# Kernel optimization log

Measured on AMD Instinct MI355X. Metric: run time of the kernel, lower is better.

## Reference

```python
import jax, jax.numpy as jnp
import numpy as np

B, N, H, DH, CZ = 1, 768, 16, 32, 128
D = H * DH  # 512
EPS = 1e-5


def layer_norm(x, w, b):
    mu = jnp.mean(x, axis=-1, keepdims=True)
    var = jnp.var(x, axis=-1, keepdims=True)
    return (x - mu) * jax.lax.rsqrt(var + EPS) * w + b


def setup_inputs() -> dict:
    key = jax.random.key(0)
    ks = jax.random.split(key, 10)
    sc = 0.02
    return {
        "s": jax.random.normal(ks[0], (B, N, D), jnp.float32),
        "z": jax.random.normal(ks[1], (B, N, N, CZ), jnp.float32),
        "norm_s_w": jnp.ones((D,), jnp.float32),
        "norm_s_b": jnp.zeros((D,), jnp.float32),
        "q_w": jax.random.normal(ks[2], (D, D), jnp.float32) * sc,
        "q_b": jax.random.normal(ks[3], (D,), jnp.float32) * sc,
        "k_w": jax.random.normal(ks[4], (D, D), jnp.float32) * sc,
        "v_w": jax.random.normal(ks[5], (D, D), jnp.float32) * sc,
        "g_w": jax.random.normal(ks[6], (D, D), jnp.float32) * sc,
        "zn_w": jnp.ones((CZ,), jnp.float32),
        "zn_b": jnp.zeros((CZ,), jnp.float32),
        "z_w": jax.random.normal(ks[7], (CZ, H), jnp.float32) * sc,
        "o_w": jax.random.normal(ks[8], (D, D), jnp.float32) * sc,
    }


def reference(s, z, norm_s_w, norm_s_b, q_w, q_b, k_w, v_w, g_w, zn_w, zn_b, z_w, o_w):
    # initial_norm on s
    s_n = layer_norm(s, norm_s_w, norm_s_b)
    # QKV projections (q has bias, k/v do not)
    q = (s_n @ q_w + q_b).reshape(B, N, H, DH)
    k = (s_n @ k_w).reshape(B, N, H, DH)
    v = (s_n @ v_w).reshape(B, N, H, DH)
    # attention scores [B, H, N, N]
    scores = jnp.einsum("bihd,bjhd->bhij", q, k) * (DH ** -0.5)
    # pair bias: layernorm(z) then linear c_z -> H, permute to [B, H, N, N]
    z_bias = layer_norm(z, zn_w, zn_b) @ z_w            # [B, N, N, H]
    z_bias = jnp.transpose(z_bias, (0, 3, 1, 2))         # [B, H, N, N]
    a = jax.nn.softmax(scores + z_bias, axis=-1)
    # attend
    o = jnp.einsum("bhij,bjhd->bihd", a, v).reshape(B, N, D)
    # sigmoid gate from normed s
    g = jax.nn.sigmoid(s_n @ g_w)
    # output projection
    return (o * g) @ o_w
```

## Files before the change

### kernel.cpp

```cpp
#include <hip/hip_runtime.h>
#include <hip/hip_bf16.h>

typedef float f32x4 __attribute__((ext_vector_type(4)));
typedef short bf16x8 __attribute__((ext_vector_type(8)));
typedef unsigned short u16;

#define NTOK 768
#define DMOD 512
#define NH   16
#define DH   32
#define CZd  128
#define NN   (768*768)

static __device__ __forceinline__ u16 f2bf(float f) {
  __hip_bfloat16 h = __float2bfloat16(f);
  return __builtin_bit_cast(u16, h);
}
static __device__ __forceinline__ float bf2f(u16 u) {
  unsigned int x = ((unsigned int)u) << 16;
  return __builtin_bit_cast(float, x);
}

__global__ __launch_bounds__(256) void prep_kernel(
    const float* __restrict__ s, const float* __restrict__ nsw, const float* __restrict__ nsb,
    const float* __restrict__ qw, const float* __restrict__ kw, const float* __restrict__ vw,
    const float* __restrict__ gw, const float* __restrict__ ow,
    const float* __restrict__ z, const float* __restrict__ znw, const float* __restrict__ znb,
    const float* __restrict__ zwp,
    u16* __restrict__ wbf, u16* __restrict__ snb, u16* __restrict__ biasb) {
  __shared__ char SM[18432];
  int bid = blockIdx.x;
  int t = threadIdx.x;

  if (bid < 1280) {
    float (*tbuf)[33] = (float(*)[33])SM;
    int seg = bid / 256;
    int tile = bid % 256;
    int k0 = (tile / 16) * 32;
    int n0 = (tile % 16) * 32;
    const float* src = seg==0?qw: seg==1?kw: seg==2?vw: seg==3?gw: ow;
    u16* out = wbf + (size_t)seg * (DMOD*DMOD);
    int tr  = t / 8;
    int tc4 = (t % 8) * 4;
    float4 v = *(const float4*)(src + (size_t)(k0+tr)*DMOD + n0 + tc4);
    tbuf[tr][tc4+0]=v.x; tbuf[tr][tc4+1]=v.y; tbuf[tr][tc4+2]=v.z; tbuf[tr][tc4+3]=v.w;
    __syncthreads();
    int nr  = t / 8;
    int kc4 = (t % 8) * 4;
    ushort4 o;
    o.x = f2bf(tbuf[kc4+0][nr]);
    o.y = f2bf(tbuf[kc4+1][nr]);
    o.z = f2bf(tbuf[kc4+2][nr]);
    o.w = f2bf(tbuf[kc4+3][nr]);
    *(ushort4*)(out + (size_t)(n0+nr)*DMOD + k0 + kc4) = o;
    return;
  }

  if (bid < 1472) {
    int i = (bid - 1280)*4 + (t >> 6);
    int lane = t & 63;
    const float* row = s + (size_t)i*DMOD + lane*8;
    float4 a0 = *(const float4*)(row);
    float4 a1 = *(const float4*)(row + 4);
    float sum = a0.x+a0.y+a0.z+a0.w + a1.x+a1.y+a1.z+a1.w;
    float sq  = a0.x*a0.x+a0.y*a0.y+a0.z*a0.z+a0.w*a0.w
              + a1.x*a1.x+a1.y*a1.y+a1.z*a1.z+a1.w*a1.w;
    #pragma unroll
    for (int mk=1; mk<64; mk<<=1) { sum += __shfl_xor(sum,mk); sq += __shfl_xor(sq,mk); }
    float mu  = sum * (1.f/512.f);
    float var = sq  * (1.f/512.f) - mu*mu;
    float rs  = rsqrtf(var + 1e-5f);
    float4 w0 = *(const float4*)(nsw + lane*8);
    float4 w1 = *(const float4*)(nsw + lane*8 + 4);
    float4 b0 = *(const float4*)(nsb + lane*8);
    float4 b1 = *(const float4*)(nsb + lane*8 + 4);
    bf16x8 o;
    o[0]=(short)f2bf((a0.x-mu)*rs*w0.x+b0.x);
    o[1]=(short)f2bf((a0.y-mu)*rs*w0.y+b0.y);
    o[2]=(short)f2bf((a0.z-mu)*rs*w0.z+b0.z);
    o[3]=(short)f2bf((a0.w-mu)*rs*w0.w+b0.w);
    o[4]=(short)f2bf((a1.x-mu)*rs*w1.x+b1.x);
    o[5]=(short)f2bf((a1.y-mu)*rs*w1.y+b1.y);
    o[6]=(short)f2bf((a1.z-mu)*rs*w1.z+b1.z);
    o[7]=(short)f2bf((a1.w-mu)*rs*w1.w+b1.w);
    *(bf16x8*)(snb + (size_t)i*DMOD + lane*8) = o;
    return;
  }

  u16*   zt   = (u16*)SM;
  float* znws = (float*)(SM + 17408);
  float* znbs = (float*)(SM + 17920);
  int zb = bid - 1472;
  int i = zb / 12, j0 = (zb % 12) * 64;
  int lane = t & 63, wv = t >> 6;
  int c16 = lane & 15, c4 = lane >> 4;
  if (t < 128) znws[t] = znw[t];
  else znbs[t-128] = znb[t-128];
  int pp = t >> 2, qq = t & 3;
  const float* zr = z + ((size_t)i*NTOK + (j0+pp))*CZd + qq*32;
  float4 xv[8];
  #pragma unroll
  for (int it=0; it<8; it++) xv[it] = *(const float4*)(zr + it*4);
  bf16x8 bfr[4];
  #pragma unroll
  for (int ks=0; ks<4; ks++) {
    #pragma unroll
    for (int jj=0; jj<8; jj++)
      bfr[ks][jj] = (short)f2bf(zwp[(ks*32 + c4*8 + jj)*16 + c16]);
  }
  float sum = 0.f, sq = 0.f;
  #pragma unroll
  for (int it=0; it<8; it++) {
    float4 v = xv[it];
    sum += v.x+v.y+v.z+v.w;
    sq  += v.x*v.x+v.y*v.y+v.z*v.z+v.w*v.w;
  }
  sum += __shfl_xor(sum,1); sq += __shfl_xor(sq,1);
  sum += __shfl_xor(sum,2); sq += __shfl_xor(sq,2);
  float mu  = sum*(1.f/128.f);
  float var = sq *(1.f/128.f) - mu*mu;
  float rs  = rsqrtf(var + 1e-5f);
  __syncthreads();
  #pragma unroll
  for (int it=0; it<8; it+=2) {
    bf16x8 ov;
    #pragma unroll
    for (int hf=0; hf<2; hf++) {
      float4 v  = xv[it+hf];
      float4 w4 = *(const float4*)(znws + qq*32 + (it+hf)*4);
      float4 b4 = *(const float4*)(znbs + qq*32 + (it+hf)*4);
      ov[hf*4+0] = (short)f2bf((v.x-mu)*rs*w4.x + b4.x);
      ov[hf*4+1] = (short)f2bf((v.y-mu)*rs*w4.y + b4.y);
      ov[hf*4+2] = (short)f2bf((v.z-mu)*rs*w4.z + b4.z);
      ov[hf*4+3] = (short)f2bf((v.w-mu)*rs*w4.w + b4.w);
    }
    *(bf16x8*)(zt + pp*136 + qq*32 + it*4) = ov;
  }
  __syncthreads();
  f32x4 acc = {0,0,0,0};
  #pragma unroll
  for (int ks=0; ks<4; ks++) {
    bf16x8 af = *(const bf16x8*)(zt + (wv*16 + c16)*136 + ks*32 + c4*8);
    acc = __builtin_amdgcn_mfma_f32_16x16x32_bf16(af, bfr[ks], acc, 0,0,0);
  }
  int jl = j0 + wv*16 + c4*4;
  u16* bp = biasb + (size_t)c16*NN + (size_t)i*NTOK + jl;
  ushort4 st;
  st.x = f2bf(acc[0]); st.y = f2bf(acc[1]); st.z = f2bf(acc[2]); st.w = f2bf(acc[3]);
  *(ushort4*)bp = st;
}

__global__ __launch_bounds__(256) void qkvg_kernel(
    const u16* __restrict__ sn, const u16* __restrict__ wts, const float* __restrict__ qb,
    u16* __restrict__ qo, u16* __restrict__ ko, u16* __restrict__ vTo, float* __restrict__ go) {
  __shared__ u16 As[64*40];
  __shared__ u16 Bs[64*40];
  int bid = blockIdx.x;
  int mb = bid % 12, nb = bid / 12;
  int wsel = nb >> 3, n0 = (nb & 7) * 64, m0 = mb * 64;
  const u16* wt = wts + (size_t)wsel * (DMOD*DMOD);
  int t = threadIdx.x, lane = t & 63, wv = t >> 6;
  int wm = (wv >> 1) * 32, wn = (wv & 1) * 32;
  int c16 = lane & 15, c4 = lane >> 4;
  int ar = t >> 2, ac = t & 3;
  f32x4 acc00={0,0,0,0}, acc01={0,0,0,0}, acc10={0,0,0,0}, acc11={0,0,0,0};
  for (int k0 = 0; k0 < DMOD; k0 += 32) {
    bf16x8 av = *(const bf16x8*)(sn + (size_t)(m0+ar)*DMOD + k0 + ac*8);
    bf16x8 bv = *(const bf16x8*)(wt + (size_t)(n0+ar)*DMOD + k0 + ac*8);
    __syncthreads();
    *(bf16x8*)(As + ar*40 + ac*8) = av;
    *(bf16x8*)(Bs + ar*40 + ac*8) = bv;
    __syncthreads();
    bf16x8 a0 = *(const bf16x8*)(As + (wm + c16)*40      + c4*8);
    bf16x8 a1 = *(const bf16x8*)(As + (wm + 16 + c16)*40 + c4*8);
    bf16x8 b0 = *(const bf16x8*)(Bs + (wn + c16)*40      + c4*8);
    bf16x8 b1 = *(const bf16x8*)(Bs + (wn + 16 + c16)*40 + c4*8);
    acc00 = __builtin_amdgcn_mfma_f32_16x16x32_bf16(a0,b0,acc00,0,0,0);
    acc01 = __builtin_amdgcn_mfma_f32_16x16x32_bf16(a0,b1,acc01,0,0,0);
    acc10 = __builtin_amdgcn_mfma_f32_16x16x32_bf16(a1,b0,acc10,0,0,0);
    acc11 = __builtin_amdgcn_mfma_f32_16x16x32_bf16(a1,b1,acc11,0,0,0);
  }
  int r0 = c4*4;
  #pragma unroll
  for (int am=0; am<2; am++) {
    #pragma unroll
    for (int bn=0; bn<2; bn++) {
      f32x4 acc = am==0 ? (bn==0?acc00:acc01) : (bn==0?acc10:acc11);
      #pragma unroll
      for (int rr=0; rr<4; rr++) {
        int i = m0 + wm + am*16 + r0 + rr;
        int n = n0 + wn + bn*16 + c16;
        float val = acc[rr];
        if (wsel == 0)      { val += qb[n]; qo[(size_t)i*DMOD + n] = f2bf(val); }
        else if (wsel == 1) { ko[(size_t)i*DMOD + n] = f2bf(val); }
        else if (wsel == 2) { vTo[(size_t)n*NTOK + i] = f2bf(val); }
        else                { go[(size_t)i*DMOD + n] = 1.f/(1.f + expf(-val)); }
      }
    }
  }
}

__global__ __launch_bounds__(64) void attn_kernel(
    const u16* __restrict__ qm, const u16* __restrict__ km, const u16* __restrict__ vTm,
    const u16* __restrict__ bias, const float* __restrict__ gm, u16* __restrict__ og) {
  __shared__ u16 Bt[16*72];
  __shared__ u16 Pt[16*72];
  int h  = blockIdx.x & 15;
  int i0 = (blockIdx.x >> 4) * 16;
  int t = threadIdx.x;
  int c16 = t & 15, c4 = t >> 4, r0 = c4 * 4;
  bf16x8 qf = *(const bf16x8*)(qm + (size_t)(i0 + c16)*DMOD + h*DH + c4*8);
  f32x4 o0 = {0,0,0,0}, o1 = {0,0,0,0};
  float ls[4] = {0.f,0.f,0.f,0.f};
  const float scale = 0.17677669529663687f;
  const u16* bbase = bias + (size_t)h*NN + (size_t)i0*NTOK;
  int br = t >> 3;
  int bc = (t & 7) * 8;
  for (int j0 = 0; j0 < NTOK; j0 += 64) {
    bf16x8 bv0 = *(const bf16x8*)(bbase + (size_t)br*NTOK     + j0 + bc);
    bf16x8 bv1 = *(const bf16x8*)(bbase + (size_t)(br+8)*NTOK + j0 + bc);
    bf16x8 kf0 = *(const bf16x8*)(km + (size_t)(j0 +  0 + c16)*DMOD + h*DH + c4*8);
    bf16x8 kf1 = *(const bf16x8*)(km + (size_t)(j0 + 16 + c16)*DMOD + h*DH + c4*8);
    bf16x8 kf2 = *(const bf16x8*)(km + (size_t)(j0 + 32 + c16)*DMOD + h*DH + c4*8);
    bf16x8 kf3 = *(const bf16x8*)(km + (size_t)(j0 + 48 + c16)*DMOD + h*DH + c4*8);
    *(bf16x8*)(Bt + br*72 + bc)     = bv0;
    *(bf16x8*)(Bt + (br+8)*72 + bc) = bv1;
    f32x4 zz = {0,0,0,0};
    f32x4 s0 = __builtin_amdgcn_mfma_f32_16x16x32_bf16(qf,kf0,zz,0,0,0);
    f32x4 s1 = __builtin_amdgcn_mfma_f32_16x16x32_bf16(qf,kf1,zz,0,0,0);
    f32x4 s2 = __builtin_amdgcn_mfma_f32_16x16x32_bf16(qf,kf2,zz,0,0,0);
    f32x4 s3 = __builtin_amdgcn_mfma_f32_16x16x32_bf16(qf,kf3,zz,0,0,0);
    #pragma unroll
    for (int rr=0; rr<4; rr++) {
      int row = (r0 + rr) * 72;
      float p0 = __expf(s0[rr]*scale + bf2f(Bt[row + 0*16 + c16]));
      float p1 = __expf(s1[rr]*scale + bf2f(Bt[row + 1*16 + c16]));
      float p2 = __expf(s2[rr]*scale + bf2f(Bt[row + 2*16 + c16]));
      float p3 = __expf(s3[rr]*scale + bf2f(Bt[row + 3*16 + c16]));
      ls[rr] += p0 + p1 + p2 + p3;
      Pt[row + 0*16 + c16] = f2bf(p0);
      Pt[row + 1*16 + c16] = f2bf(p1);
      Pt[row + 2*16 + c16] = f2bf(p2);
      Pt[row + 3*16 + c16] = f2bf(p3);
    }
    #pragma unroll
    for (int ks=0; ks<2; ks++) {
      bf16x8 pf = *(const bf16x8*)(Pt + c16*72 + ks*32 + c4*8);
      bf16x8 v0 = *(const bf16x8*)(vTm + (size_t)(h*DH + c16)*NTOK      + j0 + ks*32 + c4*8);
      bf16x8 v1 = *(const bf16x8*)(vTm + (size_t)(h*DH + 16 + c16)*NTOK + j0 + ks*32 + c4*8);
      o0 = __builtin_amdgcn_mfma_f32_16x16x32_bf16(pf, v0, o0, 0,0,0);
      o1 = __builtin_amdgcn_mfma_f32_16x16x32_bf16(pf, v1, o1, 0,0,0);
    }
  }
  #pragma unroll
  for (int rr=0; rr<4; rr++) {
    float l = ls[rr];
    l += __shfl_xor(l,1); l += __shfl_xor(l,2); l += __shfl_xor(l,4); l += __shfl_xor(l,8);
    float inv = 1.f/l;
    int i = i0 + r0 + rr;
    float g0 = gm[(size_t)i*DMOD + h*DH + c16];
    float g1 = gm[(size_t)i*DMOD + h*DH + 16 + c16];
    og[(size_t)i*DMOD + h*DH + c16]      = f2bf(o0[rr]*inv*g0);
    og[(size_t)i*DMOD + h*DH + 16 + c16] = f2bf(o1[rr]*inv*g1);
  }
}

__global__ __launch_bounds__(256) void out_kernel(
    const u16* __restrict__ og, const u16* __restrict__ owT, float* __restrict__ out) {
  __shared__ u16 As[64*40];
  __shared__ u16 Bs[64*40];
  int bid = blockIdx.x;
  int mb = bid % 12, nb = bid / 12;
  int m0 = mb*64, n0 = nb*64;
  int t = threadIdx.x, lane = t & 63, wv = t >> 6;
  int wm = (wv >> 1) * 32, wn = (wv & 1) * 32;
  int c16 = lane & 15, c4 = lane >> 4;
  int ar = t >> 2, ac = t & 3;
  f32x4 acc00={0,0,0,0}, acc01={0,0,0,0}, acc10={0,0,0,0}, acc11={0,0,0,0};
  for (int k0 = 0; k0 < DMOD; k0 += 32) {
    bf16x8 av = *(const bf16x8*)(og  + (size_t)(m0+ar)*DMOD + k0 + ac*8);
    bf16x8 bv = *(const bf16x8*)(owT + (size_t)(n0+ar)*DMOD + k0 + ac*8);
    __syncthreads();
    *(bf16x8*)(As + ar*40 + ac*8) = av;
    *(bf16x8*)(Bs + ar*40 + ac*8) = bv;
    __syncthreads();
    bf16x8 a0 = *(const bf16x8*)(As + (wm + c16)*40      + c4*8);
    bf16x8 a1 = *(const bf16x8*)(As + (wm + 16 + c16)*40 + c4*8);
    bf16x8 b0 = *(const bf16x8*)(Bs + (wn + c16)*40      + c4*8);
    bf16x8 b1 = *(const bf16x8*)(Bs + (wn + 16 + c16)*40 + c4*8);
    acc00 = __builtin_amdgcn_mfma_f32_16x16x32_bf16(a0,b0,acc00,0,0,0);
    acc01 = __builtin_amdgcn_mfma_f32_16x16x32_bf16(a0,b1,acc01,0,0,0);
    acc10 = __builtin_amdgcn_mfma_f32_16x16x32_bf16(a1,b0,acc10,0,0,0);
    acc11 = __builtin_amdgcn_mfma_f32_16x16x32_bf16(a1,b1,acc11,0,0,0);
  }
  int r0 = c4*4;
  #pragma unroll
  for (int am=0; am<2; am++) {
    #pragma unroll
    for (int bn=0; bn<2; bn++) {
      f32x4 acc = am==0 ? (bn==0?acc00:acc01) : (bn==0?acc10:acc11);
      #pragma unroll
      for (int rr=0; rr<4; rr++)
        out[(size_t)(m0 + wm + am*16 + r0 + rr)*DMOD + n0 + wn + bn*16 + c16] = acc[rr];
    }
  }
}

extern "C" void kernel_launch(void* const* d_in, const int* in_sizes, int n_in,
                              void* d_out, int out_size, void* d_ws, size_t ws_size,
                              hipStream_t stream) {
  const float* s   = (const float*)d_in[0];
  const float* z   = (const float*)d_in[1];
  const float* nsw = (const float*)d_in[2];
  const float* nsb = (const float*)d_in[3];
  const float* qw  = (const float*)d_in[4];
  const float* qb  = (const float*)d_in[5];
  const float* kw  = (const float*)d_in[6];
  const float* vw  = (const float*)d_in[7];
  const float* gw  = (const float*)d_in[8];
  const float* znw = (const float*)d_in[9];
  const float* znb = (const float*)d_in[10];
  const float* zw  = (const float*)d_in[11];
  const float* ow  = (const float*)d_in[12];
  float* out = (float*)d_out;

  char* p = (char*)d_ws;
  u16* w_bf    = (u16*)p;  p += (size_t)5*DMOD*DMOD*2;
  u16* sn_bf   = (u16*)p;  p += (size_t)NTOK*DMOD*2;
  u16* q_bf    = (u16*)p;  p += (size_t)NTOK*DMOD*2;
  u16* k_bf    = (u16*)p;  p += (size_t)NTOK*DMOD*2;
  u16* vT_bf   = (u16*)p;  p += (size_t)NTOK*DMOD*2;
  float* g_f   = (float*)p; p += (size_t)NTOK*DMOD*4;
  u16* og_bf   = (u16*)p;  p += (size_t)NTOK*DMOD*2;
  u16* bias_bf = (u16*)p;  p += (size_t)NH*NN*2;

  prep_kernel<<<dim3(10688), dim3(256), 0, stream>>>(
      s, nsw, nsb, qw, kw, vw, gw, ow, z, znw, znb, zw, w_bf, sn_bf, bias_bf);
  qkvg_kernel<<<dim3(384), dim3(256), 0, stream>>>(sn_bf, w_bf, qb, q_bf, k_bf, vT_bf, g_f);
  attn_kernel<<<dim3(768), dim3(64), 0, stream>>>(q_bf, k_bf, vT_bf, bias_bf, g_f, og_bf);
  out_kernel<<<dim3(96), dim3(256), 0, stream>>>(og_bf, w_bf + (size_t)4*DMOD*DMOD, out);
}
```

Before: 113.5 us.

## Split attention keys across four waves, shrink GEMM tiles, coalesce z loads

The attention kernel now runs four waves per (head, 16-row) block. Each wave covers a quarter of the key range, and the partial outputs and row sums are combined through shared memory before gating. The QKVG and output GEMMs use 32-row tiles, which doubles the block count to spread work across more CUs. The z layernorm load is remapped so each 32-lane group reads one contiguous 128-channel row, with per-row stats reduced by shuffles. These changes trade more blocks and an extra cross-wave reduction for higher parallelism and better coalescing.

```diff
diff --git a/kernel.cpp b/kernel.cpp
--- a/kernel.cpp
+++ b/kernel.cpp
@@ -96,11 +96,13 @@
   int c16 = lane & 15, c4 = lane >> 4;
   if (t < 128) znws[t] = znw[t];
   else znbs[t-128] = znb[t-128];
-  int pp = t >> 2, qq = t & 3;
-  const float* zr = z + ((size_t)i*NTOK + (j0+pp))*CZd + qq*32;
+  int rsub = t >> 5;
+  int ch4  = (t & 31) * 4;
+  const float* ztile = z + ((size_t)i*NTOK + j0)*CZd;
   float4 xv[8];
   #pragma unroll
-  for (int it=0; it<8; it++) xv[it] = *(const float4*)(zr + it*4);
+  for (int it=0; it<8; it++)
+    xv[it] = *(const float4*)(ztile + (size_t)(it*8 + rsub)*CZd + ch4);
   bf16x8 bfr[4];
   #pragma unroll
   for (int ks=0; ks<4; ks++) {
@@ -108,33 +110,31 @@
     for (int jj=0; jj<8; jj++)
       bfr[ks][jj] = (short)f2bf(zwp[(ks*32 + c4*8 + jj)*16 + c16]);
   }
-  float sum = 0.f, sq = 0.f;
+  float mu8[8], rs8[8];
   #pragma unroll
   for (int it=0; it<8; it++) {
     float4 v = xv[it];
-    sum += v.x+v.y+v.z+v.w;
-    sq  += v.x*v.x+v.y*v.y+v.z*v.z+v.w*v.w;
-  }
-  sum += __shfl_xor(sum,1); sq += __shfl_xor(sq,1);
-  sum += __shfl_xor(sum,2); sq += __shfl_xor(sq,2);
-  float mu  = sum*(1.f/128.f);
-  float var = sq *(1.f/128.f) - mu*mu;
-  float rs  = rsqrtf(var + 1e-5f);
+    float sum = v.x+v.y+v.z+v.w;
+    float sq  = v.x*v.x+v.y*v.y+v.z*v.z+v.w*v.w;
+    #pragma unroll
+    for (int mk=1; mk<32; mk<<=1) { sum += __shfl_xor(sum,mk); sq += __shfl_xor(sq,mk); }
+    float mu = sum*(1.f/128.f);
+    mu8[it] = mu;
+    rs8[it] = rsqrtf(sq*(1.f/128.f) - mu*mu + 1e-5f);
+  }
   __syncthreads();
-  #pragma unroll
-  for (int it=0; it<8; it+=2) {
-    bf16x8 ov;
-    #pragma unroll
-    for (int hf=0; hf<2; hf++) {
-      float4 v  = xv[it+hf];
-      float4 w4 = *(const float4*)(znws + qq*32 + (it+hf)*4);
-      float4 b4 = *(const float4*)(znbs + qq*32 + (it+hf)*4);
-      ov[hf*4+0] = (short)f2bf((v.x-mu)*rs*w4.x + b4.x);
-      ov[hf*4+1] = (short)f2bf((v.y-mu)*rs*w4.y + b4.y);
-      ov[hf*4+2] = (short)f2bf((v.z-mu)*rs*w4.z + b4.z);
-      ov[hf*4+3] = (short)f2bf((v.w-mu)*rs*w4.w + b4.w);
-    }
-    *(bf16x8*)(zt + pp*136 + qq*32 + it*4) = ov;
+  float4 w4 = *(const float4*)(znws + ch4);
+  float4 b4 = *(const float4*)(znbs + ch4);
+  #pragma unroll
+  for (int it=0; it<8; it++) {
+    float4 v = xv[it];
+    float mu = mu8[it], rs = rs8[it];
+    ushort4 o;
+    o.x = f2bf((v.x-mu)*rs*w4.x + b4.x);
+    o.y = f2bf((v.y-mu)*rs*w4.y + b4.y);
+    o.z = f2bf((v.z-mu)*rs*w4.z + b4.z);
+    o.w = f2bf((v.w-mu)*rs*w4.w + b4.w);
+    *(ushort4*)(zt + (it*8 + rsub)*136 + ch4) = o;
   }
   __syncthreads();
   f32x4 acc = {0,0,0,0};
@@ -153,78 +153,78 @@
 __global__ __launch_bounds__(256) void qkvg_kernel(
     const u16* __restrict__ sn, const u16* __restrict__ wts, const float* __restrict__ qb,
     u16* __restrict__ qo, u16* __restrict__ ko, u16* __restrict__ vTo, float* __restrict__ go) {
-  __shared__ u16 As[64*40];
+  __shared__ u16 As[32*40];
   __shared__ u16 Bs[64*40];
   int bid = blockIdx.x;
-  int mb = bid % 12, nb = bid / 12;
-  int wsel = nb >> 3, n0 = (nb & 7) * 64, m0 = mb * 64;
+  int mb = bid % 24, nb = bid / 24;
+  int wsel = nb >> 3, n0 = (nb & 7) * 64, m0 = mb * 32;
   const u16* wt = wts + (size_t)wsel * (DMOD*DMOD);
   int t = threadIdx.x, lane = t & 63, wv = t >> 6;
-  int wm = (wv >> 1) * 32, wn = (wv & 1) * 32;
+  int wm = (wv >> 1) * 16, wn = (wv & 1) * 32;
   int c16 = lane & 15, c4 = lane >> 4;
-  int ar = t >> 2, ac = t & 3;
-  f32x4 acc00={0,0,0,0}, acc01={0,0,0,0}, acc10={0,0,0,0}, acc11={0,0,0,0};
+  int sr = t >> 2, sc = t & 3;
+  f32x4 acc0={0,0,0,0}, acc1={0,0,0,0};
   for (int k0 = 0; k0 < DMOD; k0 += 32) {
-    bf16x8 av = *(const bf16x8*)(sn + (size_t)(m0+ar)*DMOD + k0 + ac*8);
-    bf16x8 bv = *(const bf16x8*)(wt + (size_t)(n0+ar)*DMOD + k0 + ac*8);
-    __syncthreads();
-    *(bf16x8*)(As + ar*40 + ac*8) = av;
-    *(bf16x8*)(Bs + ar*40 + ac*8) = bv;
-    __syncthreads();
-    bf16x8 a0 = *(const bf16x8*)(As + (wm + c16)*40      + c4*8);
-    bf16x8 a1 = *(const bf16x8*)(As + (wm + 16 + c16)*40 + c4*8);
+    bf16x8 av;
+    if (t < 128) av = *(const bf16x8*)(sn + (size_t)(m0+sr)*DMOD + k0 + sc*8);
+    bf16x8 bv = *(const bf16x8*)(wt + (size_t)(n0+sr)*DMOD + k0 + sc*8);
+    __syncthreads();
+    if (t < 128) *(bf16x8*)(As + sr*40 + sc*8) = av;
+    *(bf16x8*)(Bs + sr*40 + sc*8) = bv;
+    __syncthreads();
+    bf16x8 a  = *(const bf16x8*)(As + (wm + c16)*40      + c4*8);
     bf16x8 b0 = *(const bf16x8*)(Bs + (wn + c16)*40      + c4*8);
     bf16x8 b1 = *(const bf16x8*)(Bs + (wn + 16 + c16)*40 + c4*8);
-    acc00 = __builtin_amdgcn_mfma_f32_16x16x32_bf16(a0,b0,acc00,0,0,0);
-    acc01 = __builtin_amdgcn_mfma_f32_16x16x32_bf16(a0,b1,acc01,0,0,0);
-    acc10 = __builtin_amdgcn_mfma_f32_16x16x32_bf16(a1,b0,acc10,0,0,0);
-    acc11 = __builtin_amdgcn_mfma_f32_16x16x32_bf16(a1,b1,acc11,0,0,0);
+    acc0 = __builtin_amdgcn_mfma_f32_16x16x32_bf16(a,b0,acc0,0,0,0);
+    acc1 = __builtin_amdgcn_mfma_f32_16x16x32_bf16(a,b1,acc1,0,0,0);
   }
   int r0 = c4*4;
   #pragma unroll
-  for (int am=0; am<2; am++) {
-    #pragma unroll
-    for (int bn=0; bn<2; bn++) {
-      f32x4 acc = am==0 ? (bn==0?acc00:acc01) : (bn==0?acc10:acc11);
-      #pragma unroll
-      for (int rr=0; rr<4; rr++) {
-        int i = m0 + wm + am*16 + r0 + rr;
-        int n = n0 + wn + bn*16 + c16;
-        float val = acc[rr];
-        if (wsel == 0)      { val += qb[n]; qo[(size_t)i*DMOD + n] = f2bf(val); }
-        else if (wsel == 1) { ko[(size_t)i*DMOD + n] = f2bf(val); }
-        else if (wsel == 2) { vTo[(size_t)n*NTOK + i] = f2bf(val); }
-        else                { go[(size_t)i*DMOD + n] = 1.f/(1.f + expf(-val)); }
-      }
+  for (int bn=0; bn<2; bn++) {
+    f32x4 acc = bn==0?acc0:acc1;
+    #pragma unroll
+    for (int rr=0; rr<4; rr++) {
+      int i = m0 + wm + r0 + rr;
+      int n = n0 + wn + bn*16 + c16;
+      float val = acc[rr];
+      if (wsel == 0)      { val += qb[n]; qo[(size_t)i*DMOD + n] = f2bf(val); }
+      else if (wsel == 1) { ko[(size_t)i*DMOD + n] = f2bf(val); }
+      else if (wsel == 2) { vTo[(size_t)n*NTOK + i] = f2bf(val); }
+      else                { go[(size_t)i*DMOD + n] = 1.f/(1.f + expf(-val)); }
     }
   }
 }
 
-__global__ __launch_bounds__(64) void attn_kernel(
+__global__ __launch_bounds__(256) void attn_kernel(
     const u16* __restrict__ qm, const u16* __restrict__ km, const u16* __restrict__ vTm,
     const u16* __restrict__ bias, const float* __restrict__ gm, u16* __restrict__ og) {
-  __shared__ u16 Bt[16*72];
-  __shared__ u16 Pt[16*72];
+  __shared__ u16 Bt[4][16*72];
+  __shared__ u16 Pt[4][16*72];
+  __shared__ float OS[4][16][33];
+  __shared__ float LS[4][16];
   int h  = blockIdx.x & 15;
   int i0 = (blockIdx.x >> 4) * 16;
-  int t = threadIdx.x;
-  int c16 = t & 15, c4 = t >> 4, r0 = c4 * 4;
+  int t = threadIdx.x, lane = t & 63, wv = t >> 6;
+  int c16 = lane & 15, c4 = lane >> 4, r0 = c4 * 4;
   bf16x8 qf = *(const bf16x8*)(qm + (size_t)(i0 + c16)*DMOD + h*DH + c4*8);
   f32x4 o0 = {0,0,0,0}, o1 = {0,0,0,0};
   float ls[4] = {0.f,0.f,0.f,0.f};
   const float scale = 0.17677669529663687f;
   const u16* bbase = bias + (size_t)h*NN + (size_t)i0*NTOK;
-  int br = t >> 3;
-  int bc = (t & 7) * 8;
-  for (int j0 = 0; j0 < NTOK; j0 += 64) {
+  int br = lane >> 3;
+  int bc = (lane & 7) * 8;
+  u16* bt = &Bt[wv][0];
+  u16* pt = &Pt[wv][0];
+  for (int jj = 0; jj < 3; jj++) {
+    int j0 = wv*192 + jj*64;
     bf16x8 bv0 = *(const bf16x8*)(bbase + (size_t)br*NTOK     + j0 + bc);
     bf16x8 bv1 = *(const bf16x8*)(bbase + (size_t)(br+8)*NTOK + j0 + bc);
     bf16x8 kf0 = *(const bf16x8*)(km + (size_t)(j0 +  0 + c16)*DMOD + h*DH + c4*8);
     bf16x8 kf1 = *(const bf16x8*)(km + (size_t)(j0 + 16 + c16)*DMOD + h*DH + c4*8);
     bf16x8 kf2 = *(const bf16x8*)(km + (size_t)(j0 + 32 + c16)*DMOD + h*DH + c4*8);
     bf16x8 kf3 = *(const bf16x8*)(km + (size_t)(j0 + 48 + c16)*DMOD + h*DH + c4*8);
-    *(bf16x8*)(Bt + br*72 + bc)     = bv0;
-    *(bf16x8*)(Bt + (br+8)*72 + bc) = bv1;
+    *(bf16x8*)(bt + br*72 + bc)     = bv0;
+    *(bf16x8*)(bt + (br+8)*72 + bc) = bv1;
     f32x4 zz = {0,0,0,0};
     f32x4 s0 = __builtin_amdgcn_mfma_f32_16x16x32_bf16(qf,kf0,zz,0,0,0);
     f32x4 s1 = __builtin_amdgcn_mfma_f32_16x16x32_bf16(qf,kf1,zz,0,0,0);
@@ -233,19 +233,19 @@
     #pragma unroll
     for (int rr=0; rr<4; rr++) {
       int row = (r0 + rr) * 72;
-      float p0 = __expf(s0[rr]*scale + bf2f(Bt[row + 0*16 + c16]));
-      float p1 = __expf(s1[rr]*scale + bf2f(Bt[row + 1*16 + c16]));
-      float p2 = __expf(s2[rr]*scale + bf2f(Bt[row + 2*16 + c16]));
-      float p3 = __expf(s3[rr]*scale + bf2f(Bt[row + 3*16 + c16]));
+      float p0 = __expf(s0[rr]*scale + bf2f(bt[row + 0*16 + c16]));
+      float p1 = __expf(s1[rr]*scale + bf2f(bt[row + 1*16 + c16]));
+      float p2 = __expf(s2[rr]*scale + bf2f(bt[row + 2*16 + c16]));
+      float p3 = __expf(s3[rr]*scale + bf2f(bt[row + 3*16 + c16]));
       ls[rr] += p0 + p1 + p2 + p3;
-      Pt[row + 0*16 + c16] = f2bf(p0);
-      Pt[row + 1*16 + c16] = f2bf(p1);
-      Pt[row + 2*16 + c16] = f2bf(p2);
-      Pt[row + 3*16 + c16] = f2bf(p3);
+      pt[row + 0*16 + c16] = f2bf(p0);
+      pt[row + 1*16 + c16] = f2bf(p1);
+      pt[row + 2*16 + c16] = f2bf(p2);
+      pt[row + 3*16 + c16] = f2bf(p3);
     }
     #pragma unroll
     for (int ks=0; ks<2; ks++) {
-      bf16x8 pf = *(const bf16x8*)(Pt + c16*72 + ks*32 + c4*8);
+      bf16x8 pf = *(const bf16x8*)(pt + c16*72 + ks*32 + c4*8);
       bf16x8 v0 = *(const bf16x8*)(vTm + (size_t)(h*DH + c16)*NTOK      + j0 + ks*32 + c4*8);
       bf16x8 v1 = *(const bf16x8*)(vTm + (size_t)(h*DH + 16 + c16)*NTOK + j0 + ks*32 + c4*8);
       o0 = __builtin_amdgcn_mfma_f32_16x16x32_bf16(pf, v0, o0, 0,0,0);
@@ -256,53 +256,56 @@
   for (int rr=0; rr<4; rr++) {
     float l = ls[rr];
     l += __shfl_xor(l,1); l += __shfl_xor(l,2); l += __shfl_xor(l,4); l += __shfl_xor(l,8);
-    float inv = 1.f/l;
-    int i = i0 + r0 + rr;
-    float g0 = gm[(size_t)i*DMOD + h*DH + c16];
-    float g1 = gm[(size_t)i*DMOD + h*DH + 16 + c16];
-    og[(size_t)i*DMOD + h*DH + c16]      = f2bf(o0[rr]*inv*g0);
-    og[(size_t)i*DMOD + h*DH + 16 + c16] = f2bf(o1[rr]*inv*g1);
+    OS[wv][r0+rr][c16]      = o0[rr];
+    OS[wv][r0+rr][16 + c16] = o1[rr];
+    if (c16 == 0) LS[wv][r0+rr] = l;
+  }
+  __syncthreads();
+  #pragma unroll
+  for (int u=0; u<2; u++) {
+    int idx = t + u*256;
+    int row = idx >> 5, d = idx & 31;
+    float osum = OS[0][row][d] + OS[1][row][d] + OS[2][row][d] + OS[3][row][d];
+    float lsum = LS[0][row] + LS[1][row] + LS[2][row] + LS[3][row];
+    int i = i0 + row;
+    float g = gm[(size_t)i*DMOD + h*DH + d];
+    og[(size_t)i*DMOD + h*DH + d] = f2bf(osum/lsum*g);
   }
 }
 
 __global__ __launch_bounds__(256) void out_kernel(
     const u16* __restrict__ og, const u16* __restrict__ owT, float* __restrict__ out) {
-  __shared__ u16 As[64*40];
+  __shared__ u16 As[32*40];
   __shared__ u16 Bs[64*40];
   int bid = blockIdx.x;
-  int mb = bid % 12, nb = bid / 12;
-  int m0 = mb*64, n0 = nb*64;
+  int mb = bid % 24, nb = bid / 24;
+  int m0 = mb*32, n0 = nb*64;
   int t = threadIdx.x, lane = t & 63, wv = t >> 6;
-  int wm = (wv >> 1) * 32, wn = (wv & 1) * 32;
+  int wm = (wv >> 1) * 16, wn = (wv & 1) * 32;
   int c16 = lane & 15, c4 = lane >> 4;
-  int ar = t >> 2, ac = t & 3;
-  f32x4 acc00={0,0,0,0}, acc01={0,0,0,0}, acc10={0,0,0,0}, acc11={0,0,0,0};
+  int sr = t >> 2, sc = t & 3;
+  f32x4 acc0={0,0,0,0}, acc1={0,0,0,0};
   for (int k0 = 0; k0 < DMOD; k0 += 32) {
-    bf16x8 av = *(const bf16x8*)(og  + (size_t)(m0+ar)*DMOD + k0 + ac*8);
-    bf16x8 bv = *(const bf16x8*)(owT + (size_t)(n0+ar)*DMOD + k0 + ac*8);
-    __syncthreads();
-    *(bf16x8*)(As + ar*40 + ac*8) = av;
-    *(bf16x8*)(Bs + ar*40 + ac*8) = bv;
-    __syncthreads();
-    bf16x8 a0 = *(const bf16x8*)(As + (wm + c16)*40      + c4*8);
-    bf16x8 a1 = *(const bf16x8*)(As + (wm + 16 + c16)*40 + c4*8);
+    bf16x8 av;
+    if (t < 128) av = *(const bf16x8*)(og + (size_t)(m0+sr)*DMOD + k0 + sc*8);
+    bf16x8 bv = *(const bf16x8*)(owT + (size_t)(n0+sr)*DMOD + k0 + sc*8);
+    __syncthreads();
+    if (t < 128) *(bf16x8*)(As + sr*40 + sc*8) = av;
+    *(bf16x8*)(Bs + sr*40 + sc*8) = bv;
+    __syncthreads();
+    bf16x8 a  = *(const bf16x8*)(As + (wm + c16)*40      + c4*8);
     bf16x8 b0 = *(const bf16x8*)(Bs + (wn + c16)*40      + c4*8);
     bf16x8 b1 = *(const bf16x8*)(Bs + (wn + 16 + c16)*40 + c4*8);
-    acc00 = __builtin_amdgcn_mfma_f32_16x16x32_bf16(a0,b0,acc00,0,0,0);
-    acc01 = __builtin_amdgcn_mfma_f32_16x16x32_bf16(a0,b1,acc01,0,0,0);
-    acc10 = __builtin_amdgcn_mfma_f32_16x16x32_bf16(a1,b0,acc10,0,0,0);
-    acc11 = __builtin_amdgcn_mfma_f32_16x16x32_bf16(a1,b1,acc11,0,0,0);
+    acc0 = __builtin_amdgcn_mfma_f32_16x16x32_bf16(a,b0,acc0,0,0,0);
+    acc1 = __builtin_amdgcn_mfma_f32_16x16x32_bf16(a,b1,acc1,0,0,0);
   }
   int r0 = c4*4;
   #pragma unroll
-  for (int am=0; am<2; am++) {
-    #pragma unroll
-    for (int bn=0; bn<2; bn++) {
-      f32x4 acc = am==0 ? (bn==0?acc00:acc01) : (bn==0?acc10:acc11);
-      #pragma unroll
-      for (int rr=0; rr<4; rr++)
-        out[(size_t)(m0 + wm + am*16 + r0 + rr)*DMOD + n0 + wn + bn*16 + c16] = acc[rr];
-    }
+  for (int bn=0; bn<2; bn++) {
+    f32x4 acc = bn==0?acc0:acc1;
+    #pragma unroll
+    for (int rr=0; rr<4; rr++)
+      out[(size_t)(m0 + wm + r0 + rr)*DMOD + n0 + wn + bn*16 + c16] = acc[rr];
   }
 }
 
@@ -336,7 +339,7 @@
 
   prep_kernel<<<dim3(10688), dim3(256), 0, stream>>>(
       s, nsw, nsb, qw, kw, vw, gw, ow, z, znw, znb, zw, w_bf, sn_bf, bias_bf);
-  qkvg_kernel<<<dim3(384), dim3(256), 0, stream>>>(sn_bf, w_bf, qb, q_bf, k_bf, vT_bf, g_f);
-  attn_kernel<<<dim3(768), dim3(64), 0, stream>>>(q_bf, k_bf, vT_bf, bias_bf, g_f, og_bf);
-  out_kernel<<<dim3(96), dim3(256), 0, stream>>>(og_bf, w_bf + (size_t)4*DMOD*DMOD, out);
-}
+  qkvg_kernel<<<dim3(768), dim3(256), 0, stream>>>(sn_bf, w_bf, qb, q_bf, k_bf, vT_bf, g_f);
+  attn_kernel<<<dim3(768), dim3(256), 0, stream>>>(q_bf, k_bf, vT_bf, bias_bf, g_f, og_bf);
+  out_kernel<<<dim3(192), dim3(256), 0, stream>>>(og_bf, w_bf + (size_t)4*DMOD*DMOD, out);
+}
```

New measurement: 101.1 us. -10.9%, faster.
